# Performance work log

Measured on AMD Instinct MI355X. Metric: run time of the kernel, lower is better.

The kernel has to match this reference:

```python
import jax, jax.numpy as jnp
import numpy as np

IMAGE_SIZE = (256, 704)
FEATURE_SIZE = (32, 88)
XBOUND = (-54.0, 54.0, 0.3)
YBOUND = (-54.0, 54.0, 0.3)
ZBOUND = (-10.0, 10.0, 20.0)
DBOUND = (1.0, 60.0, 1.0)


def _grid_params():
    bounds = [XBOUND, YBOUND, ZBOUND]
    dx = jnp.array([b[2] for b in bounds], jnp.float32)
    bx = jnp.array([b[0] + b[2] / 2.0 for b in bounds], jnp.float32)
    nx = [int((b[1] - b[0]) / b[2]) for b in bounds]  # [360, 360, 1]
    return dx, bx, nx


def _frustum():
    iH, iW = IMAGE_SIZE
    fH, fW = FEATURE_SIZE
    ds = jnp.arange(DBOUND[0], DBOUND[1], DBOUND[2], dtype=jnp.float32)  # [D]
    D = ds.shape[0]
    xs = jnp.linspace(0.0, iW - 1, fW, dtype=jnp.float32)
    ys = jnp.linspace(0.0, iH - 1, fH, dtype=jnp.float32)
    xs_b = jnp.broadcast_to(xs[None, None, :], (D, fH, fW))
    ys_b = jnp.broadcast_to(ys[None, :, None], (D, fH, fW))
    ds_b = jnp.broadcast_to(ds[:, None, None], (D, fH, fW))
    return jnp.stack([xs_b, ys_b, ds_b], axis=-1)  # [D, fH, fW, 3]


def setup_inputs() -> dict:
    key = jax.random.key(0)
    k1, k2, k3, k4 = jax.random.split(key, 4)
    B, N, C = 2, 6, 80
    fH, fW = FEATURE_SIZE
    D = _frustum().shape[0]  # 59
    feats = jax.random.normal(k1, (B, N, D, fH, fW, C), dtype=jnp.float32)
    img_trans = 0.5 * jax.random.normal(k2, (B, N, 3), dtype=jnp.float32)
    img_scale = 0.9 + 0.2 * jax.random.uniform(k3, (B, N), dtype=jnp.float32)
    # camera-intrinsic-like lidar2img: diag(focal, focal, 1, 1) + small noise,
    # guaranteed well-conditioned so jnp.linalg.inv is stable
    base = jnp.diag(jnp.array([500.0, 500.0, 1.0, 1.0], jnp.float32))
    lidar2img = base[None, None] + 0.1 * jax.random.normal(k4, (B, N, 4, 4), dtype=jnp.float32)
    return {"feats": feats, "img_trans": img_trans, "img_scale": img_scale, "lidar2img": lidar2img}


def reference(feats, img_trans, img_scale, lidar2img):
    B, N, D, H, W, C = feats.shape
    dx, bx, nx = _grid_params()
    NX, NY, NZ = nx
    fr = _frustum()  # [D, H, W, 3]

    # ---- get_geometry (eval mode: no pcd augmentations) ----
    pts = fr[None, None] + img_trans[:, :, None, None, None, :]  # [B,N,D,H,W,3]
    d = pts[..., 2:3]
    xy = pts[..., :2] / img_scale[:, :, None, None, None, None]
    ones = jnp.ones_like(d)
    p4 = jnp.concatenate([xy * d, d, ones], axis=-1)  # [B,N,D,H,W,4]
    img2lidar = jnp.linalg.inv(lidar2img)  # [B,N,4,4]
    geom = jnp.einsum('bnij,bndhwj->bndhwi', img2lidar, p4)[..., :3]

    # ---- bev_pool: voxelize + masked scatter-sum into dense BEV grid ----
    # torch .long() truncates toward zero; float->int astype in jax matches
    vox = ((geom - (bx - dx / 2.0)) / dx).astype(jnp.int32)  # [B,N,D,H,W,3]
    vox = vox.reshape(B, -1, 3)
    x = feats.reshape(B, -1, C)
    mask = ((vox[..., 0] >= 0) & (vox[..., 0] < NX)
            & (vox[..., 1] >= 0) & (vox[..., 1] < NY)
            & (vox[..., 2] >= 0) & (vox[..., 2] < NZ))
    # flat index into [B, Z, X, Y] grid
    flat = (vox[..., 2] * NX + vox[..., 0]) * NY + vox[..., 1]
    flat = flat + jnp.arange(B, dtype=jnp.int32)[:, None] * (NZ * NX * NY)
    flat = jnp.where(mask, flat, 0)  # masked points carry zero features -> harmless
    xm = x * mask[..., None].astype(x.dtype)
    grid = jax.ops.segment_sum(xm.reshape(-1, C), flat.reshape(-1),
                               num_segments=B * NZ * NX * NY)
    grid = grid.reshape(B, NZ, NX, NY, C)
    # bev_pool returns [B, C, Z, X, Y]; cat(unbind(dim=2), 1) -> [B, Z*C, X, Y]
    final = jnp.transpose(grid, (0, 1, 4, 2, 3)).reshape(B, NZ * C, NX, NY)
    return final
```

## Files before the change

kernel.cpp:

```cpp
#include <hip/hip_runtime.h>
#include <math.h>

#define B_ 2
#define N_ 6
#define D_ 59
#define FH 32
#define FW 88
#define C_ 80
#define NX 360
#define NY 360
#define P_PER_B (N_*D_*FH*FW)
#define NPTS (B_*P_PER_B)
#define NCELL (NX*NY)
#define NC (B_*NCELL)
#define NBLK 254
#define NCP (NBLK*1024)
#define OUT4 (B_*C_*NCELL/4)
#define SMAX 48
#define CHK 192
#define MAXCHK (NC + NPTS/CHK)
#define TOTBLK 2048
#define BBLK 512
#define SBLK (TOTBLK - BBLK)

__device__ int   g_code[NPTS];
__device__ __align__(16) int g_cnt[NCP];
__device__ int   g_escan[NCP];
__device__ int   g_bsum[NBLK];
__device__ int   g_offs[NC+1];
__device__ int   g_cur[NC];
__device__ __align__(16) int g_plist[NPTS];
__device__ int   g_nS, g_nB;
__device__ int   g_nS2, g_nB2;
__device__ int2  g_cellS[NC];
__device__ int2  g_chunkB[MAXCHK];

__global__ void k_geomz(const float* __restrict__ itrans,
                        const float* __restrict__ iscale,
                        const float* __restrict__ l2i,
                        float* __restrict__ out) {
#pragma clang fp contract(off)
  __shared__ float sinv[B_*N_*16];
  int tid = threadIdx.x;
  int p = blockIdx.x*256 + tid;

  const float4 z4 = make_float4(0.f,0.f,0.f,0.f);
  #pragma unroll
  for (int s=0; s<3; ++s) {
    int u = p + s*NPTS;
    if (u < OUT4) ((float4*)out)[u] = z4;
  }

  if (tid < B_*N_) {
    int m = tid;
    double a[4][4], inv[4][4];
    for (int r=0;r<4;r++) for (int j=0;j<4;j++){
      a[r][j] = (double)l2i[m*16+r*4+j];
      inv[r][j] = (r==j)?1.0:0.0;
    }
    for (int k=0;k<4;k++){
      int pv=k; double mx=fabs(a[k][k]);
      for (int r=k+1;r<4;r++){ double v=fabs(a[r][k]); if (v>mx){mx=v;pv=r;} }
      if (pv!=k){
        for (int j=0;j<4;j++){
          double t=a[k][j]; a[k][j]=a[pv][j]; a[pv][j]=t;
          t=inv[k][j]; inv[k][j]=inv[pv][j]; inv[pv][j]=t;
        }
      }
      double pi = 1.0/a[k][k];
      for (int j=0;j<4;j++){ a[k][j]*=pi; inv[k][j]*=pi; }
      for (int r=0;r<4;r++) if (r!=k){
        double f=a[r][k];
        for (int j=0;j<4;j++){ a[r][j]-=f*a[k][j]; inv[r][j]-=f*inv[k][j]; }
      }
    }
    for (int r=0;r<4;r++) for (int j=0;j<4;j++)
      sinv[m*16+r*4+j] = (float)inv[r][j];
  }
  __syncthreads();

  int b  = p / P_PER_B;
  int r  = p - b*P_PER_B;
  int n  = r / (D_*FH*FW);
  int r2 = r - n*(D_*FH*FW);
  int d  = r2 / (FH*FW);
  int r3 = r2 - d*(FH*FW);
  int h  = r3 / FW;
  int w  = r3 - h*FW;
  int bn = b*N_ + n;

  float xw = (float)((double)w * (703.0/87.0));
  float yh = (float)((double)h * (255.0/31.0));
  float dd = (float)(d + 1);

  float t0 = itrans[bn*3+0], t1 = itrans[bn*3+1], t2 = itrans[bn*3+2];
  float s  = iscale[bn];

  float px = xw + t0, py = yh + t1, pd = dd + t2;
  float x0 = px / s, x1 = py / s;
  float p0 = x0*pd, p1 = x1*pd, p2 = pd;

  const float* iv = &sinv[bn*16];
  float gx = ((iv[0]*p0 + iv[1]*p1) + iv[2]*p2)  + iv[3]*1.0f;
  float gy = ((iv[4]*p0 + iv[5]*p1) + iv[6]*p2)  + iv[7]*1.0f;
  float gz = ((iv[8]*p0 + iv[9]*p1) + iv[10]*p2) + iv[11]*1.0f;

  int vx = (int)((gx + 54.0f) / 0.3f);
  int vy = (int)((gy + 54.0f) / 0.3f);
  int vz = (int)((gz + 10.0f) / 20.0f);

  bool ok = (vx>=0) & (vx<NX) & (vy>=0) & (vy<NY) & (vz>=0) & (vz<1);
  int code = ok ? (b*NCELL + vx*NY + vy) : -1;
  g_code[p] = code;

  int lane = tid & 63;
  int prev = __shfl_up(code, 1);
  bool leader = (lane == 0) || (code != prev);
  unsigned long long m = __ballot(leader);
  if (leader && code >= 0) {
    unsigned long long above = (lane < 63) ? (m >> (lane+1)) : 0ULL;
    int len = above ? __ffsll(above) : (64 - lane);
    atomicAdd(&g_cnt[code], len);
  }
}

__global__ void __launch_bounds__(1024) k_scanA() {
  __shared__ int sd[1024];
  int t = threadIdx.x;
  int i = blockIdx.x*1024 + t;
  int v = g_cnt[i];
  sd[t] = v;
  for (int off=1; off<1024; off<<=1) {
    __syncthreads();
    int x = (t >= off) ? sd[t-off] : 0;
    __syncthreads();
    sd[t] += x;
  }
  g_escan[i] = sd[t] - v;
  if (t == 1023) g_bsum[blockIdx.x] = sd[1023];
}

__global__ void __launch_bounds__(1024) k_scanC() {
  __shared__ int sb[256];
  int t = threadIdx.x, bid = blockIdx.x;
  if (t < 256) sb[t] = (t < NBLK) ? g_bsum[t] : 0;
  for (int off=1; off<256; off<<=1) {
    __syncthreads();
    int x = 0;
    if (t >= off && t < 256) x = sb[t-off];
    __syncthreads();
    if (t < 256) sb[t] += x;
  }
  __syncthreads();
  int bpre = (bid > 0) ? sb[bid-1] : 0;
  if (bid == 0 && t == 0) g_offs[NC] = sb[NBLK-1];

  int i = bid*1024 + t;
  bool inb = (i < NC);
  int o = 0, len = 0;
  if (inb) {
    o = g_escan[i] + bpre;
    g_offs[i] = o;
    g_cur[i]  = o;
    len = g_cnt[i];
  }
  int lane = t & 63;
  bool isS = inb && (len > 0) && (len <= SMAX);
  unsigned long long m = __ballot(isS);
  if (m) {
    int ldr = __ffsll((long long)m) - 1;
    int base = 0;
    if (lane == ldr) base = atomicAdd(&g_nS, (int)__popcll(m));
    base = __shfl(base, ldr);
    if (isS) {
      int rank = __popcll(m & ((1ULL << lane) - 1ULL));
      g_cellS[base + rank] = make_int2(i, o);
    }
  }
  if (inb && len > SMAX) {
    int nch = (len + CHK - 1) / CHK;
    int base = atomicAdd(&g_nB, nch);
    for (int k = 0; k < nch; ++k)
      g_chunkB[base + k] = make_int2(i, o + k*CHK);
  }
}

__global__ void k_fill() {
  int gid = blockIdx.x*256 + threadIdx.x;
  if (gid < NCP/4) ((int4*)g_cnt)[gid] = make_int4(0,0,0,0);
  if (gid == 0) { g_nS2 = g_nS; g_nB2 = g_nB; g_nS = 0; g_nB = 0; }

  int code = g_code[gid];
  int lane = threadIdx.x & 63;
  int prev = __shfl_up(code, 1);
  bool leader = (lane == 0) || (code != prev);
  unsigned long long m = __ballot(leader);
  unsigned long long mask_le = (lane==63) ? ~0ULL : ((1ULL << (lane+1)) - 1ULL);
  int leaderLane = 63 - __clzll(m & mask_le);
  int pos0 = 0;
  if (leader && code >= 0) {
    unsigned long long above = (lane < 63) ? (m >> (lane+1)) : 0ULL;
    int len = above ? __ffsll(above) : (64 - lane);
    pos0 = atomicAdd(&g_cur[code], len);
  }
  pos0 = __shfl(pos0, leaderLane);
  if (code >= 0) g_plist[pos0 + (lane - leaderLane)] = gid;
}

__global__ void __launch_bounds__(256) k_gather(const float* __restrict__ feats,
                                                float* __restrict__ out) {
  const float4* f4 = (const float4*)feats;
  if (blockIdx.x < BBLK) {
    int nB = g_nB2;
    int lane = threadIdx.x & 63;
    int wid = blockIdx.x*4 + (threadIdx.x >> 6);
    int grp = lane/20;
    int c4 = lane - grp*20;
    bool act = lane < 60;
    for (int it = wid; it < nB; it += BBLK*4) {
      int2 e = g_chunkB[it];
      int c = e.x, s0 = e.y;
      int o0 = g_offs[c], o1 = g_offs[c+1];
      int s1 = min(s0 + CHK, o1);
      float ax=0.f, ay=0.f, az=0.f, aw=0.f;
      if (act) {
        int j = s0 + grp;
        for (; j + 9 < s1; j += 12) {
          int p0=g_plist[j], p1=g_plist[j+3], p2=g_plist[j+6], p3=g_plist[j+9];
          float4 v0=f4[(size_t)p0*20+c4], v1=f4[(size_t)p1*20+c4];
          float4 v2=f4[(size_t)p2*20+c4], v3=f4[(size_t)p3*20+c4];
          ax += v0.x+v1.x+v2.x+v3.x;
          ay += v0.y+v1.y+v2.y+v3.y;
          az += v0.z+v1.z+v2.z+v3.z;
          aw += v0.w+v1.w+v2.w+v3.w;
        }
        for (; j < s1; j += 3) {
          int p = g_plist[j];
          float4 v = f4[(size_t)p*20+c4];
          ax+=v.x; ay+=v.y; az+=v.z; aw+=v.w;
        }
      }
      float bx=__shfl(ax,c4+20), by=__shfl(ay,c4+20), bz=__shfl(az,c4+20), bw=__shfl(aw,c4+20);
      float cx=__shfl(ax,c4+40), cy=__shfl(ay,c4+40), cz=__shfl(az,c4+40), cw=__shfl(aw,c4+40);
      if (lane < 20) {
        ax += bx + cx; ay += by + cy; az += bz + cz; aw += bw + cw;
        int b = c / NCELL;
        int xy = c - b*NCELL;
        float* dst = out + (size_t)(b*C_ + c4*4)*NCELL + xy;
        if (o1 - o0 <= CHK) {
          dst[0]       = ax;
          dst[NCELL]   = ay;
          dst[2*NCELL] = az;
          dst[3*NCELL] = aw;
        } else {
          atomicAdd(dst,         ax);
          atomicAdd(dst+NCELL,   ay);
          atomicAdd(dst+2*NCELL, az);
          atomicAdd(dst+3*NCELL, aw);
        }
      }
    }
  } else {
    int nS = g_nS2;
    int tot = nS*20;
    for (int i = (blockIdx.x - BBLK)*256 + threadIdx.x; i < tot; i += SBLK*256) {
      int ci = i/20;
      int c4 = i - ci*20;
      int2 e = g_cellS[ci];
      int c = e.x, o0 = e.y;
      int o1 = g_offs[c+1];
      float ax=0.f, ay=0.f, az=0.f, aw=0.f;
      int j = o0;
      for (; j + 8 <= o1; j += 8) {
        int p0=g_plist[j],   p1=g_plist[j+1], p2=g_plist[j+2], p3=g_plist[j+3];
        int p4=g_plist[j+4], p5=g_plist[j+5], p6=g_plist[j+6], p7=g_plist[j+7];
        float4 v0=f4[(size_t)p0*20+c4], v1=f4[(size_t)p1*20+c4];
        float4 v2=f4[(size_t)p2*20+c4], v3=f4[(size_t)p3*20+c4];
        float4 v4=f4[(size_t)p4*20+c4], v5=f4[(size_t)p5*20+c4];
        float4 v6=f4[(size_t)p6*20+c4], v7=f4[(size_t)p7*20+c4];
        ax += (v0.x+v1.x)+(v2.x+v3.x)+(v4.x+v5.x)+(v6.x+v7.x);
        ay += (v0.y+v1.y)+(v2.y+v3.y)+(v4.y+v5.y)+(v6.y+v7.y);
        az += (v0.z+v1.z)+(v2.z+v3.z)+(v4.z+v5.z)+(v6.z+v7.z);
        aw += (v0.w+v1.w)+(v2.w+v3.w)+(v4.w+v5.w)+(v6.w+v7.w);
      }
      for (; j < o1; ++j) {
        int p = g_plist[j];
        float4 v = f4[(size_t)p*20+c4];
        ax+=v.x; ay+=v.y; az+=v.z; aw+=v.w;
      }
      int b = c / NCELL;
      int xy = c - b*NCELL;
      float* dst = out + (size_t)(b*C_ + c4*4)*NCELL + xy;
      dst[0]       = ax;
      dst[NCELL]   = ay;
      dst[2*NCELL] = az;
      dst[3*NCELL] = aw;
    }
  }
}

extern "C" void kernel_launch(void* const* d_in, const int* in_sizes, int n_in,
                              void* d_out, int out_size, void* d_ws, size_t ws_size,
                              hipStream_t stream) {
  const float* feats  = (const float*)d_in[0];
  const float* itrans = (const float*)d_in[1];
  const float* iscale = (const float*)d_in[2];
  const float* l2i    = (const float*)d_in[3];
  float* out = (float*)d_out;

  k_geomz<<<NPTS/256, 256, 0, stream>>>(itrans, iscale, l2i, out);
  k_scanA<<<NBLK, 1024, 0, stream>>>();
  k_scanC<<<NBLK, 1024, 0, stream>>>();
  k_fill<<<NPTS/256, 256, 0, stream>>>();
  k_gather<<<TOTBLK, 256, 0, stream>>>(feats, out);
}
```

Baseline: 133.0 us.

## Replace global prefix scan with per-wave atomic allocation and pack cell metadata

Replaces the two-kernel exclusive scan with a single kernel that does a wave-level prefix sum and reserves contiguous plist space per wave through a global atomic counter. Segment lengths are packed into the cell and chunk descriptors, so the gather no longer reads an offsets array. The small-cell threshold and chunk size shrink, the big-cell loop is unrolled wider, and the small-cell loop is made branch-free with masked FMAs over fixed groups of 8. Cells are no longer in sorted order in plist, which is fine for a sum, but the masked loop issues extra clamped loads for padding elements.

```diff
diff --git a/kernel.cpp b/kernel.cpp
--- a/kernel.cpp
+++ b/kernel.cpp
@@ -16,20 +16,18 @@
 #define NBLK 254
 #define NCP (NBLK*1024)
 #define OUT4 (B_*C_*NCELL/4)
-#define SMAX 48
-#define CHK 192
-#define MAXCHK (NC + NPTS/CHK)
+#define SMAX 32
+#define CHK 96
+#define MAXCHK (NC/4 + NPTS/CHK)
 #define TOTBLK 2048
 #define BBLK 512
 #define SBLK (TOTBLK - BBLK)
 
 __device__ int   g_code[NPTS];
 __device__ __align__(16) int g_cnt[NCP];
-__device__ int   g_escan[NCP];
-__device__ int   g_bsum[NBLK];
-__device__ int   g_offs[NC+1];
 __device__ int   g_cur[NC];
 __device__ __align__(16) int g_plist[NPTS];
+__device__ int   g_total;
 __device__ int   g_nS, g_nB;
 __device__ int   g_nS2, g_nB2;
 __device__ int2  g_cellS[NC];
@@ -124,71 +122,53 @@
   }
 }
 
-__global__ void __launch_bounds__(1024) k_scanA() {
-  __shared__ int sd[1024];
-  int t = threadIdx.x;
-  int i = blockIdx.x*1024 + t;
-  int v = g_cnt[i];
-  sd[t] = v;
-  for (int off=1; off<1024; off<<=1) {
-    __syncthreads();
-    int x = (t >= off) ? sd[t-off] : 0;
-    __syncthreads();
-    sd[t] += x;
-  }
-  g_escan[i] = sd[t] - v;
-  if (t == 1023) g_bsum[blockIdx.x] = sd[1023];
-}
-
-__global__ void __launch_bounds__(1024) k_scanC() {
-  __shared__ int sb[256];
+__global__ void __launch_bounds__(1024) k_alloc() {
   int t = threadIdx.x, bid = blockIdx.x;
-  if (t < 256) sb[t] = (t < NBLK) ? g_bsum[t] : 0;
-  for (int off=1; off<256; off<<=1) {
-    __syncthreads();
-    int x = 0;
-    if (t >= off && t < 256) x = sb[t-off];
-    __syncthreads();
-    if (t < 256) sb[t] += x;
-  }
-  __syncthreads();
-  int bpre = (bid > 0) ? sb[bid-1] : 0;
-  if (bid == 0 && t == 0) g_offs[NC] = sb[NBLK-1];
-
   int i = bid*1024 + t;
   bool inb = (i < NC);
-  int o = 0, len = 0;
-  if (inb) {
-    o = g_escan[i] + bpre;
-    g_offs[i] = o;
-    g_cur[i]  = o;
-    len = g_cnt[i];
-  }
+  int len = inb ? g_cnt[i] : 0;
   int lane = t & 63;
+
+  int pre = len;
+  #pragma unroll
+  for (int off=1; off<64; off<<=1) {
+    int x = __shfl_up(pre, off);
+    if (lane >= off) pre += x;
+  }
+  int wtot = __shfl(pre, 63);
+  int wbase = 0;
+  if (lane == 63 && wtot > 0) wbase = atomicAdd(&g_total, wtot);
+  wbase = __shfl(wbase, 63);
+  int base = wbase + pre - len;
+  if (inb && len > 0) g_cur[i] = base;
+
   bool isS = inb && (len > 0) && (len <= SMAX);
   unsigned long long m = __ballot(isS);
   if (m) {
     int ldr = __ffsll((long long)m) - 1;
-    int base = 0;
-    if (lane == ldr) base = atomicAdd(&g_nS, (int)__popcll(m));
-    base = __shfl(base, ldr);
+    int cbase = 0;
+    if (lane == ldr) cbase = atomicAdd(&g_nS, (int)__popcll(m));
+    cbase = __shfl(cbase, ldr);
     if (isS) {
       int rank = __popcll(m & ((1ULL << lane) - 1ULL));
-      g_cellS[base + rank] = make_int2(i, o);
+      g_cellS[cbase + rank] = make_int2(i | (len << 18), base);
     }
   }
   if (inb && len > SMAX) {
     int nch = (len + CHK - 1) / CHK;
-    int base = atomicAdd(&g_nB, nch);
-    for (int k = 0; k < nch; ++k)
-      g_chunkB[base + k] = make_int2(i, o + k*CHK);
+    int cb = atomicAdd(&g_nB, nch);
+    int sole = (nch == 1) ? 1 : 0;
+    for (int k = 0; k < nch; ++k) {
+      int clen = min(CHK, len - k*CHK);
+      g_chunkB[cb + k] = make_int2(i | (clen << 18) | (sole << 30), base + k*CHK);
+    }
   }
 }
 
 __global__ void k_fill() {
   int gid = blockIdx.x*256 + threadIdx.x;
   if (gid < NCP/4) ((int4*)g_cnt)[gid] = make_int4(0,0,0,0);
-  if (gid == 0) { g_nS2 = g_nS; g_nB2 = g_nB; g_nS = 0; g_nB = 0; }
+  if (gid == 0) { g_nS2 = g_nS; g_nB2 = g_nB; g_nS = 0; g_nB = 0; g_total = 0; }
 
   int code = g_code[gid];
   int lane = threadIdx.x & 63;
@@ -219,24 +199,27 @@
     bool act = lane < 60;
     for (int it = wid; it < nB; it += BBLK*4) {
       int2 e = g_chunkB[it];
-      int c = e.x, s0 = e.y;
-      int o0 = g_offs[c], o1 = g_offs[c+1];
-      int s1 = min(s0 + CHK, o1);
+      int c    = e.x & 0x3FFFF;
+      int clen = (e.x >> 18) & 0x7F;
+      int sole = (e.x >> 30) & 1;
+      int s0 = e.y;
+      int s1 = s0 + clen;
       float ax=0.f, ay=0.f, az=0.f, aw=0.f;
       if (act) {
         int j = s0 + grp;
-        for (; j + 9 < s1; j += 12) {
-          int p0=g_plist[j], p1=g_plist[j+3], p2=g_plist[j+6], p3=g_plist[j+9];
-          float4 v0=f4[(size_t)p0*20+c4], v1=f4[(size_t)p1*20+c4];
-          float4 v2=f4[(size_t)p2*20+c4], v3=f4[(size_t)p3*20+c4];
-          ax += v0.x+v1.x+v2.x+v3.x;
-          ay += v0.y+v1.y+v2.y+v3.y;
-          az += v0.z+v1.z+v2.z+v3.z;
-          aw += v0.w+v1.w+v2.w+v3.w;
+        for (; j + 21 < s1; j += 24) {
+          int p[8];
+          #pragma unroll
+          for (int k=0;k<8;++k) p[k] = g_plist[j + 3*k];
+          float4 v[8];
+          #pragma unroll
+          for (int k=0;k<8;++k) v[k] = f4[(size_t)p[k]*20 + c4];
+          #pragma unroll
+          for (int k=0;k<8;++k) { ax+=v[k].x; ay+=v[k].y; az+=v[k].z; aw+=v[k].w; }
         }
         for (; j < s1; j += 3) {
           int p = g_plist[j];
-          float4 v = f4[(size_t)p*20+c4];
+          float4 v = f4[(size_t)p*20 + c4];
           ax+=v.x; ay+=v.y; az+=v.z; aw+=v.w;
         }
       }
@@ -247,7 +230,7 @@
         int b = c / NCELL;
         int xy = c - b*NCELL;
         float* dst = out + (size_t)(b*C_ + c4*4)*NCELL + xy;
-        if (o1 - o0 <= CHK) {
+        if (sole) {
           dst[0]       = ax;
           dst[NCELL]   = ay;
           dst[2*NCELL] = az;
@@ -267,26 +250,31 @@
       int ci = i/20;
       int c4 = i - ci*20;
       int2 e = g_cellS[ci];
-      int c = e.x, o0 = e.y;
-      int o1 = g_offs[c+1];
+      int c   = e.x & 0x3FFFF;
+      int len = (e.x >> 18) & 0x7F;
+      int o0  = e.y;
       float ax=0.f, ay=0.f, az=0.f, aw=0.f;
-      int j = o0;
-      for (; j + 8 <= o1; j += 8) {
-        int p0=g_plist[j],   p1=g_plist[j+1], p2=g_plist[j+2], p3=g_plist[j+3];
-        int p4=g_plist[j+4], p5=g_plist[j+5], p6=g_plist[j+6], p7=g_plist[j+7];
-        float4 v0=f4[(size_t)p0*20+c4], v1=f4[(size_t)p1*20+c4];
-        float4 v2=f4[(size_t)p2*20+c4], v3=f4[(size_t)p3*20+c4];
-        float4 v4=f4[(size_t)p4*20+c4], v5=f4[(size_t)p5*20+c4];
-        float4 v6=f4[(size_t)p6*20+c4], v7=f4[(size_t)p7*20+c4];
-        ax += (v0.x+v1.x)+(v2.x+v3.x)+(v4.x+v5.x)+(v6.x+v7.x);
-        ay += (v0.y+v1.y)+(v2.y+v3.y)+(v4.y+v5.y)+(v6.y+v7.y);
-        az += (v0.z+v1.z)+(v2.z+v3.z)+(v4.z+v5.z)+(v6.z+v7.z);
-        aw += (v0.w+v1.w)+(v2.w+v3.w)+(v4.w+v5.w)+(v6.w+v7.w);
-      }
-      for (; j < o1; ++j) {
-        int p = g_plist[j];
-        float4 v = f4[(size_t)p*20+c4];
-        ax+=v.x; ay+=v.y; az+=v.z; aw+=v.w;
+      int nb = (len + 7) >> 3;
+      for (int bi = 0; bi < nb; ++bi) {
+        int base = o0 + bi*8;
+        int rem = len - bi*8;
+        int p[8];
+        #pragma unroll
+        for (int k=0;k<8;++k) p[k] = g_plist[min(base+k, NPTS-1)];
+        float4 v[8];
+        #pragma unroll
+        for (int k=0;k<8;++k) {
+          int q = min(max(p[k],0), NPTS-1);
+          v[k] = f4[(size_t)q*20 + c4];
+        }
+        #pragma unroll
+        for (int k=0;k<8;++k) {
+          float sel = (k < rem) ? 1.f : 0.f;
+          ax = fmaf(sel, v[k].x, ax);
+          ay = fmaf(sel, v[k].y, ay);
+          az = fmaf(sel, v[k].z, az);
+          aw = fmaf(sel, v[k].w, aw);
+        }
       }
       int b = c / NCELL;
       int xy = c - b*NCELL;
@@ -309,8 +297,7 @@
   float* out = (float*)d_out;
 
   k_geomz<<<NPTS/256, 256, 0, stream>>>(itrans, iscale, l2i, out);
-  k_scanA<<<NBLK, 1024, 0, stream>>>();
-  k_scanC<<<NBLK, 1024, 0, stream>>>();
+  k_alloc<<<NBLK, 1024, 0, stream>>>();
   k_fill<<<NPTS/256, 256, 0, stream>>>();
   k_gather<<<TOTBLK, 256, 0, stream>>>(feats, out);
 }
```

Result: faster. 127.6 us (-4.1%).
